# Kernel optimization log

Measured on AMD Instinct MI355X. Metric: run time of the kernel, lower is better.

The kernel has to match this reference:

```python
import jax, jax.numpy as jnp
import numpy as np

N = 2_000_000          # number of points
BOX = 4.0              # points live in [0, BOX)^3 meters
H = 3                  # hidden_channels (hardcoded in module)
NCLASS = 20
VS_ENC = [0.02, 0.04, 0.08]
VS_DEC = [0.08, 0.04, 0.02]


def _sparse_conv(feat, pts, vs, W, bias=None, transpose=False):
    """Voxel-hashed 3x3x3 sparse conv over continuous point positions.

    feat: [N, Cin] point features; pts: [N, 3] positions; W: [3,3,3,Cin,Cout].
    Points are voxelized at voxel size vs; each output point sums, over the 27
    kernel offsets, W[off] applied to the pooled features of the neighboring
    voxel.  transpose=True flips the kernel (SparseConvTranspose).
    """
    G = int(np.ceil(BOX / vs)) + 3                     # padded grid extent
    vox = jnp.floor(pts / vs).astype(jnp.int32) + 1    # +1 pad so offsets stay in range
    flat = (vox[:, 0] * G + vox[:, 1]) * G + vox[:, 2] # [N] flat voxel id
    Cin, Cout = W.shape[3], W.shape[4]
    # scatter-pool point features into the dense voxel grid
    grid = jnp.zeros((G * G * G, Cin), feat.dtype).at[flat].add(feat)
    Wk = (W[::-1, ::-1, ::-1] if transpose else W).reshape(27, Cin, Cout)
    out = jnp.zeros((feat.shape[0], Cout), feat.dtype)
    k = 0
    for dx in (-1, 0, 1):          # static 27-offset loop (kernel taps)
        for dy in (-1, 0, 1):
            for dz in (-1, 0, 1):
                nb = flat + (dx * G + dy) * G + dz
                out = out + grid[nb] @ Wk[k]
                k += 1
    if bias is not None:
        out = out + bias
    return out


def setup_inputs() -> dict:
    key = jax.random.key(0)
    ks = jax.random.split(key, 12)
    coords = jax.random.uniform(ks[0], (3, N), jnp.float32, 0.0, BOX)
    pixel_vals = jax.random.normal(ks[1], (N, 3), jnp.float32)
    w = lambda k: jax.random.normal(k, (3, 3, 3, H, H), jnp.float32) * 0.1
    return {
        "coords": coords,
        "pixel_vals": pixel_vals,
        "w_enc1": w(ks[2]),
        "w_enc2": w(ks[3]),
        "w_enc3": w(ks[4]),
        "w_dec1": w(ks[5]), "b_dec1": jnp.zeros((H,), jnp.float32),
        "w_dec2": w(ks[6]), "b_dec2": jnp.zeros((H,), jnp.float32),
        "w_dec3": w(ks[7]), "b_dec3": jnp.zeros((H,), jnp.float32),
        "w_gen": jax.random.normal(ks[8], (H, NCLASS), jnp.float32) * 0.1,
        "b_gen": jnp.zeros((NCLASS,), jnp.float32),
    }


def reference(coords, pixel_vals, w_enc1, w_enc2, w_enc3,
              w_dec1, b_dec1, w_dec2, b_dec2, w_dec3, b_dec3,
              w_gen, b_gen):
    pts = coords.T  # [N, 3]
    out = jax.nn.relu(_sparse_conv(pixel_vals, pts, VS_ENC[0], w_enc1))
    out = jax.nn.relu(_sparse_conv(out, pts, VS_ENC[1], w_enc2))
    out = jax.nn.relu(_sparse_conv(out, pts, VS_ENC[2], w_enc3))
    out = jax.nn.relu(_sparse_conv(out, pts, VS_DEC[0], w_dec1, b_dec1, transpose=True))
    out = jax.nn.relu(_sparse_conv(out, pts, VS_DEC[1], w_dec2, b_dec2, transpose=True))
    out = jax.nn.relu(_sparse_conv(out, pts, VS_DEC[2], w_dec3, b_dec3, transpose=True))
    return out @ w_gen + b_gen
```

## Files before the change

kernel.cpp:

```cpp
#include <hip/hip_runtime.h>
#include <math.h>


static constexpr int THREADS = 256;


__global__ void __launch_bounds__(THREADS)
scatter_pack_kernel(const float* __restrict__ coords, const float* __restrict__ pv,
                    int* __restrict__ flat, unsigned long long* __restrict__ gi, int n)
{
    int i = blockIdx.x * blockDim.x + threadIdx.x;
    if (i >= n) return;
    float x = coords[i], y = coords[n + i], z = coords[2 * n + i];
    int vx = (int)floorf(x * 50.0f) + 1;
    int vy = (int)floorf(y * 50.0f) + 1;
    int vz = (int)floorf(z * 50.0f) + 1;
    int f = (vx * 203 + vy) * 203 + vz;
    flat[i] = f;
    int q0 = __float2int_rn(pv[3 * i + 0] * 512.0f) + 4096;
    int q1 = __float2int_rn(pv[3 * i + 1] * 512.0f) + 4096;
    int q2 = __float2int_rn(pv[3 * i + 2] * 512.0f) + 4096;
    unsigned long long a = (1ULL << 48)
                         | ((unsigned long long)(unsigned int)q0 << 32)
                         | ((unsigned long long)(unsigned int)q1 << 16)
                         | (unsigned long long)(unsigned int)q2;
    atomicAdd(&gi[f], a);
}

__device__ __forceinline__ void dec16(unsigned long long v,
                                      float& f0, float& f1, float& f2)
{
    int cnt = (int)(v >> 48);
    int b = cnt << 12;
    f0 = (float)((int)((v >> 32) & 0xffff) - b) * (1.0f / 512.0f);
    f1 = (float)((int)((v >> 16) & 0xffff) - b) * (1.0f / 512.0f);
    f2 = (float)((int)(v         & 0xffff) - b) * (1.0f / 512.0f);
}

__global__ void __launch_bounds__(THREADS)
conv_gi_kernel(const unsigned long long* __restrict__ gi,
               const float* __restrict__ W,
               float4* __restrict__ T,
               unsigned char* __restrict__ cnt1)
{
    constexpr int G = 203, E = 201;
    __shared__ float sW[243];
    int t = threadIdx.x;
    if (t < 243) sW[t] = W[t];
    __syncthreads();

    int i = blockIdx.x * blockDim.x + t;
    if (i >= E * E * E) return;
    unsigned ui = (unsigned)i;
    int z = (int)(ui % (unsigned)E) + 1;  unsigned q = ui / (unsigned)E;
    int y = (int)(q % (unsigned)E) + 1;
    int x = (int)(q / (unsigned)E) + 1;
    int base = (x * G + y) * G + z;

    float a0 = 0.f, a1 = 0.f, a2 = 0.f;
    float cntC = 0.f;
    #pragma unroll
    for (int dx = -1; dx <= 1; ++dx) {
        #pragma unroll
        for (int dy = -1; dy <= 1; ++dy) {
            const unsigned long long* row = gi + base + (dx * G + dy) * G;
            unsigned long long vm = row[-1], v0 = row[0], vp = row[1];
            if (dx == 0 && dy == 0) cntC = (float)(int)(v0 >> 48);
            float m0, m1, m2, c0, c1, c2, p0, p1, p2;
            dec16(vm, m0, m1, m2);
            dec16(v0, c0, c1, c2);
            dec16(vp, p0, p1, p2);
            #pragma unroll
            for (int dz = -1; dz <= 1; ++dz) {
                const float* w = &sW[(((1 + dx) * 3 + (1 + dy)) * 3 + (1 + dz)) * 9];
                float g0 = (dz < 0) ? m0 : ((dz == 0) ? c0 : p0);
                float g1 = (dz < 0) ? m1 : ((dz == 0) ? c1 : p1);
                float g2 = (dz < 0) ? m2 : ((dz == 0) ? c2 : p2);
                a0 += g0 * w[0] + g1 * w[3] + g2 * w[6];
                a1 += g0 * w[1] + g1 * w[4] + g2 * w[7];
                a2 += g0 * w[2] + g1 * w[5] + g2 * w[8];
            }
        }
    }
    T[base] = make_float4(cntC, cntC * fmaxf(a0, 0.f),
                          cntC * fmaxf(a1, 0.f), cntC * fmaxf(a2, 0.f));
    cnt1[base] = (unsigned char)min((int)cntC, 255);
}

template <int G, int E, bool FLIP, bool MULC, bool BIAS>
__global__ void __launch_bounds__(THREADS)
conv_dense_kernel(const float4* __restrict__ in, const float* __restrict__ W,
                  const float* __restrict__ bias, float4* __restrict__ out)
{
    __shared__ float sW[243];
    __shared__ float sB[3];
    int t = threadIdx.x;
    if (t < 243) sW[t] = W[t];
    if (t < 3)   sB[t] = BIAS ? bias[t] : 0.0f;
    __syncthreads();

    int i = blockIdx.x * blockDim.x + t;
    if (i >= E * E * E) return;
    unsigned ui = (unsigned)i;
    int z = (int)(ui % (unsigned)E) + 1;  unsigned q = ui / (unsigned)E;
    int y = (int)(q % (unsigned)E) + 1;
    int x = (int)(q / (unsigned)E) + 1;
    int base = (x * G + y) * G + z;

    float a0 = sB[0], a1 = sB[1], a2 = sB[2];
    float cnt = 0.0f;
    #pragma unroll
    for (int dx = -1; dx <= 1; ++dx) {
        #pragma unroll
        for (int dy = -1; dy <= 1; ++dy) {
            int r = base + (dx * G + dy) * G;
            float4 va = in[r - 1], vb = in[r], vc = in[r + 1];
            if (dx == 0 && dy == 0) cnt = vb.x;
            #pragma unroll
            for (int dz = -1; dz <= 1; ++dz) {
                const int ax = FLIP ? 1 - dx : 1 + dx;
                const int ay = FLIP ? 1 - dy : 1 + dy;
                const int az = FLIP ? 1 - dz : 1 + dz;
                const float* w = &sW[((ax * 3 + ay) * 3 + az) * 9];
                float g0, g1, g2;
                if (dz == -1)      { g0 = va.y; g1 = va.z; g2 = va.w; }
                else if (dz == 0)  { g0 = vb.y; g1 = vb.z; g2 = vb.w; }
                else               { g0 = vc.y; g1 = vc.z; g2 = vc.w; }
                a0 += g0 * w[0] + g1 * w[3] + g2 * w[6];
                a1 += g0 * w[1] + g1 * w[4] + g2 * w[7];
                a2 += g0 * w[2] + g1 * w[5] + g2 * w[8];
            }
        }
    }
    a0 = fmaxf(a0, 0.0f); a1 = fmaxf(a1, 0.0f); a2 = fmaxf(a2, 0.0f);
    if (MULC) { a0 *= cnt; a1 *= cnt; a2 *= cnt; }
    out[base] = make_float4(cnt, a0, a1, a2);
}

template <int G, int GC, bool FLIP>
__global__ void __launch_bounds__(THREADS)
conv_fpar_kernel(const unsigned char* __restrict__ cnt,
                 const float4* __restrict__ coarse,
                 const float* __restrict__ W,
                 const float* __restrict__ bias,
                 float4* __restrict__ out)
{
    constexpr int E = G - 2;
    __shared__ float sW[243];
    __shared__ float sB[3];
    int t = threadIdx.x;
    if (t < 243) sW[t] = W[t];
    if (t < 3)   sB[t] = bias[t];
    __syncthreads();

    int i = blockIdx.x * blockDim.x + t;
    if (i >= E * E * E) return;
    unsigned ui = (unsigned)i;
    int z = (int)(ui % (unsigned)E) + 1;  unsigned q = ui / (unsigned)E;
    int y = (int)(q % (unsigned)E) + 1;
    int x = (int)(q / (unsigned)E) + 1;

    int pzm = ((z - 2) >> 1) + 1;
    int pz0 = ((z - 1) >> 1) + 1;
    int pzp = (z >> 1) + 1;

    float a0 = sB[0], a1 = sB[1], a2 = sB[2];
    float cnt_c = 0.0f;

    #pragma unroll
    for (int dx = -1; dx <= 1; ++dx) {
        int gxr = x + dx;
        int px = ((gxr - 1) >> 1) + 1;
        #pragma unroll
        for (int dy = -1; dy <= 1; ++dy) {
            int gyr = y + dy;
            int py = ((gyr - 1) >> 1) + 1;
            size_t r = ((size_t)gxr * G + gyr) * G + z;
            float cm = (float)cnt[r - 1];
            float c0 = (float)cnt[r];
            float cp = (float)cnt[r + 1];
            if (dx == 0 && dy == 0) cnt_c = c0;
            const float4* crow = coarse + ((size_t)px * GC + py) * GC;
            float4 Cm = crow[pzm], C0 = crow[pz0], Cp = crow[pzp];
            #pragma unroll
            for (int dz = -1; dz <= 1; ++dz) {
                float  cc = (dz < 0) ? cm : ((dz == 0) ? c0 : cp);
                float4 C  = (dz < 0) ? Cm : ((dz == 0) ? C0 : Cp);
                const int ax = FLIP ? 1 - dx : 1 + dx;
                const int ay = FLIP ? 1 - dy : 1 + dy;
                const int az = FLIP ? 1 - dz : 1 + dz;
                const float* w = &sW[((ax * 3 + ay) * 3 + az) * 9];
                float g0 = cc * C.y, g1 = cc * C.z, g2 = cc * C.w;
                a0 += g0 * w[0] + g1 * w[3] + g2 * w[6];
                a1 += g0 * w[1] + g1 * w[4] + g2 * w[7];
                a2 += g0 * w[2] + g1 * w[5] + g2 * w[8];
            }
        }
    }
    out[((size_t)x * G + y) * G + z] =
        make_float4(cnt_c, fmaxf(a0, 0.0f), fmaxf(a1, 0.0f), fmaxf(a2, 0.0f));
}

template <int Gc, int Gf, int Mc, bool WCNT>
__global__ void __launch_bounds__(THREADS)
down4_kernel(const float4* __restrict__ fine, float4* __restrict__ coarse,
             unsigned char* __restrict__ cntc)
{
    int i = blockIdx.x * blockDim.x + threadIdx.x;
    if (i >= Mc * Mc * Mc) return;
    unsigned ui = (unsigned)i;
    int zc = (int)(ui % (unsigned)Mc) + 1;  unsigned q = ui / (unsigned)Mc;
    int yc = (int)(q % (unsigned)Mc) + 1;
    int xc = (int)(q / (unsigned)Mc) + 1;
    int xf = 2 * xc - 1, yf = 2 * yc - 1, zf = 2 * zc - 1;
    float4 s = make_float4(0, 0, 0, 0);
    #pragma unroll
    for (int a = 0; a < 2; ++a)
        #pragma unroll
        for (int b = 0; b < 2; ++b) {
            int r = ((xf + a) * Gf + (yf + b)) * Gf + zf;
            float4 u = fine[r], v = fine[r + 1];
            s.x += u.x + v.x; s.y += u.y + v.y;
            s.z += u.z + v.z; s.w += u.w + v.w;
        }
    int idx = (xc * Gc + yc) * Gc + zc;
    coarse[idx] = s;
    if (WCNT) cntc[idx] = (unsigned char)min((int)(s.x + 0.5f), 255);
}

__global__ void __launch_bounds__(THREADS)
final_head_kernel(const int* __restrict__ flat, const float4* __restrict__ yF,
                  const float* __restrict__ wg, const float* __restrict__ bg,
                  float* __restrict__ out, int n)
{
    __shared__ float sG[60], sGB[20];
    int t = threadIdx.x;
    if (t < 60) sG[t] = wg[t];
    if (t < 20) sGB[t] = bg[t];
    __syncthreads();
    int i = blockIdx.x * blockDim.x + t;
    if (i >= n) return;
    float4 v = yF[flat[i]];
    float* o = out + (size_t)i * 20;
    #pragma unroll
    for (int c = 0; c < 20; ++c)
        o[c] = v.y * sG[c] + v.z * sG[20 + c] + v.w * sG[40 + c] + sGB[c];
}


__global__ void __launch_bounds__(THREADS)
voxelize_kernel(const float* __restrict__ coords, int* __restrict__ flat,
                float inv_vs, int G, int n)
{
    int i = blockIdx.x * blockDim.x + threadIdx.x;
    if (i >= n) return;
    int vx = (int)floorf(coords[i] * inv_vs) + 1;
    int vy = (int)floorf(coords[n + i] * inv_vs) + 1;
    int vz = (int)floorf(coords[2 * n + i] * inv_vs) + 1;
    flat[i] = (vx * G + vy) * G + vz;
}

__global__ void __launch_bounds__(THREADS)
scatter_kernel(const int* __restrict__ flat, const float* __restrict__ feat,
               float* __restrict__ grid, int n)
{
    int i = blockIdx.x * blockDim.x + threadIdx.x;
    if (i >= n) return;
    int f = flat[i];
    atomicAdd(&grid[3 * f + 0], feat[3 * i + 0]);
    atomicAdd(&grid[3 * f + 1], feat[3 * i + 1]);
    atomicAdd(&grid[3 * f + 2], feat[3 * i + 2]);
}

template <bool FLIP, bool FUSE_GEN>
__global__ void __launch_bounds__(THREADS)
gather_conv_kernel(const int* __restrict__ flat, const float* __restrict__ grid,
                   const float* __restrict__ W, const float* __restrict__ bias,
                   const float* __restrict__ w_gen, const float* __restrict__ b_gen,
                   float* __restrict__ out, int G, int n)
{
    __shared__ float sW[243];
    __shared__ float sB[3];
    __shared__ float sG[60];
    __shared__ float sGB[20];
    int t = threadIdx.x;
    if (t < 243) sW[t] = W[t];
    if (t < 3)   sB[t] = bias ? bias[t] : 0.0f;
    if (FUSE_GEN) {
        if (t < 60) sG[t]  = w_gen[t];
        if (t < 20) sGB[t] = b_gen[t];
    }
    __syncthreads();
    int i = blockIdx.x * blockDim.x + t;
    if (i >= n) return;
    int f = flat[i];
    float acc0 = sB[0], acc1 = sB[1], acc2 = sB[2];
    #pragma unroll
    for (int dx = -1; dx <= 1; ++dx) {
        #pragma unroll
        for (int dy = -1; dy <= 1; ++dy) {
            int base = f + (dx * G + dy) * G - 1;
            const float* g = &grid[3 * base];
            float gv[9];
            #pragma unroll
            for (int qq = 0; qq < 9; ++qq) gv[qq] = g[qq];
            #pragma unroll
            for (int dz = -1; dz <= 1; ++dz) {
                const int a = FLIP ? (1 - dx) : (1 + dx);
                const int b = FLIP ? (1 - dy) : (1 + dy);
                const int c = FLIP ? (1 - dz) : (1 + dz);
                const float* w = &sW[((a * 3 + b) * 3 + c) * 9];
                float g0 = gv[(dz + 1) * 3 + 0];
                float g1 = gv[(dz + 1) * 3 + 1];
                float g2 = gv[(dz + 1) * 3 + 2];
                acc0 += g0 * w[0] + g1 * w[3] + g2 * w[6];
                acc1 += g0 * w[1] + g1 * w[4] + g2 * w[7];
                acc2 += g0 * w[2] + g1 * w[5] + g2 * w[8];
            }
        }
    }
    acc0 = fmaxf(acc0, 0.0f); acc1 = fmaxf(acc1, 0.0f); acc2 = fmaxf(acc2, 0.0f);
    if (FUSE_GEN) {
        float* o = out + (size_t)i * 20;
        #pragma unroll
        for (int c = 0; c < 20; ++c)
            o[c] = acc0 * sG[c] + acc1 * sG[20 + c] + acc2 * sG[40 + c] + sGB[c];
    } else {
        out[3 * i + 0] = acc0;
        out[3 * i + 1] = acc1;
        out[3 * i + 2] = acc2;
    }
}

extern "C" void kernel_launch(void* const* d_in, const int* in_sizes, int n_in,
                              void* d_out, int out_size, void* d_ws, size_t ws_size,
                              hipStream_t stream)
{
    const float* coords     = (const float*)d_in[0];
    const float* pixel_vals = (const float*)d_in[1];
    const float* w_enc1 = (const float*)d_in[2];
    const float* w_enc2 = (const float*)d_in[3];
    const float* w_enc3 = (const float*)d_in[4];
    const float* w_dec1 = (const float*)d_in[5];
    const float* b_dec1 = (const float*)d_in[6];
    const float* w_dec2 = (const float*)d_in[7];
    const float* b_dec2 = (const float*)d_in[8];
    const float* w_dec3 = (const float*)d_in[9];
    const float* b_dec3 = (const float*)d_in[10];
    const float* w_gen  = (const float*)d_in[11];
    const float* b_gen  = (const float*)d_in[12];

    const int n = in_sizes[0] / 3;
    const int blocks = (n + THREADS - 1) / THREADS;
    float* out = (float*)d_out;

    constexpr size_t SZ_BIG1 = 33461712;
    constexpr size_t SZ_G2   = 4370912;
    constexpr size_t SZ_G3   = 595512;
    const size_t nf = ((size_t)n + 3) & ~(size_t)3;
    size_t off_flat = SZ_BIG1;
    size_t off_g2   = off_flat + nf;
    size_t off_t2   = off_g2 + SZ_G2;
    size_t off_g3   = off_t2 + SZ_G2;
    size_t off_t3   = off_g3 + SZ_G3;
    size_t need     = (off_t3 + SZ_G3) * 4;
    constexpr int    FTOT  = 203 * 203 * 203;
    constexpr int    C2TOT = 103 * 103 * 103;
    constexpr size_t GI_BYTES = (size_t)FTOT * 8;
    constexpr size_t CNT1_OFF = (GI_BYTES + 255) & ~(size_t)255;
    constexpr size_t CNT2_OFF = (CNT1_OFF + (size_t)FTOT + 255) & ~(size_t)255;
    const size_t outBytes = (size_t)out_size * 4;
    bool fast = (ws_size >= need) && (outBytes >= CNT2_OFF + (size_t)C2TOT);

    if (fast) {
        float* ws    = (float*)d_ws;
        float4* big1 = (float4*)ws;
        int*    flat = (int*)(ws + off_flat);
        float4* g2   = (float4*)(ws + off_g2);
        float4* t2   = (float4*)(ws + off_t2);
        float4* g3   = (float4*)(ws + off_g3);
        float4* t3   = (float4*)(ws + off_t3);
        unsigned long long* gi = (unsigned long long*)d_out;
        unsigned char* cnt1 = (unsigned char*)d_out + CNT1_OFF;
        unsigned char* cnt2 = (unsigned char*)d_out + CNT2_OFF;

        auto nb = [](int cells) { return (cells + THREADS - 1) / THREADS; };
        constexpr int C1 = 201 * 201 * 201, C2 = 101 * 101 * 101, C3 = 51 * 51 * 51;
        constexpr int D2 = 100 * 100 * 100, D3 = 50 * 50 * 50;

        (void)hipMemsetAsync(gi, 0, GI_BYTES, stream);
        (void)hipMemsetAsync(cnt1, 0, (size_t)FTOT, stream);
        (void)hipMemsetAsync(cnt2, 0, (size_t)C2TOT, stream);
        (void)hipMemsetAsync(g2, 0, SZ_G2 * 4, stream);
        (void)hipMemsetAsync(t2, 0, SZ_G2 * 4, stream);
        (void)hipMemsetAsync(g3, 0, SZ_G3 * 4, stream);
        (void)hipMemsetAsync(t3, 0, SZ_G3 * 4, stream);

        scatter_pack_kernel<<<blocks, THREADS, 0, stream>>>(
            coords, pixel_vals, flat, gi, n);

        conv_gi_kernel<<<nb(C1), THREADS, 0, stream>>>(gi, w_enc1, big1, cnt1);
        down4_kernel<103, 203, 100, true><<<nb(D2), THREADS, 0, stream>>>(big1, g2, cnt2);

        conv_dense_kernel<103, 101, false, true, false>
            <<<nb(C2), THREADS, 0, stream>>>(g2, w_enc2, nullptr, t2);
        down4_kernel<53, 103, 50, false><<<nb(D3), THREADS, 0, stream>>>(t2, g3, nullptr);

        conv_dense_kernel<53, 51, false, true, false>
            <<<nb(C3), THREADS, 0, stream>>>(g3, w_enc3, nullptr, t3);

        conv_dense_kernel<53, 51, true, false, true>
            <<<nb(C3), THREADS, 0, stream>>>(t3, w_dec1, b_dec1, g3);

        conv_fpar_kernel<103, 53, true>
            <<<nb(C2), THREADS, 0, stream>>>(cnt2, g3, w_dec2, b_dec2, t2);

        conv_fpar_kernel<203, 103, true>
            <<<nb(C1), THREADS, 0, stream>>>(cnt1, t2, w_dec3, b_dec3, big1);

        final_head_kernel<<<blocks, THREADS, 0, stream>>>(
            flat, big1, w_gen, b_gen, out, n);
        return;
    }

    float* ws   = (float*)d_ws;
    float* grid = ws;
    int*   flat = (int*)(ws + 25096284);
    float* featA = out;
    float* featB = out + (size_t)n * 3;

    const int   G1 = 203, G2 = 103, G3 = 53;
    const float I1 = 50.0f, I2 = 25.0f, I3 = 12.5f;
    auto gridBytes = [](int G) { return (size_t)G * G * G * 3 * sizeof(float); };

    voxelize_kernel<<<blocks, THREADS, 0, stream>>>(coords, flat, I1, G1, n);
    (void)hipMemsetAsync(grid, 0, gridBytes(G1), stream);
    scatter_kernel<<<blocks, THREADS, 0, stream>>>(flat, pixel_vals, grid, n);
    gather_conv_kernel<false, false><<<blocks, THREADS, 0, stream>>>(
        flat, grid, w_enc1, nullptr, nullptr, nullptr, featA, G1, n);

    voxelize_kernel<<<blocks, THREADS, 0, stream>>>(coords, flat, I2, G2, n);
    (void)hipMemsetAsync(grid, 0, gridBytes(G2), stream);
    scatter_kernel<<<blocks, THREADS, 0, stream>>>(flat, featA, grid, n);
    gather_conv_kernel<false, false><<<blocks, THREADS, 0, stream>>>(
        flat, grid, w_enc2, nullptr, nullptr, nullptr, featB, G2, n);

    voxelize_kernel<<<blocks, THREADS, 0, stream>>>(coords, flat, I3, G3, n);
    (void)hipMemsetAsync(grid, 0, gridBytes(G3), stream);
    scatter_kernel<<<blocks, THREADS, 0, stream>>>(flat, featB, grid, n);
    gather_conv_kernel<false, false><<<blocks, THREADS, 0, stream>>>(
        flat, grid, w_enc3, nullptr, nullptr, nullptr, featA, G3, n);

    (void)hipMemsetAsync(grid, 0, gridBytes(G3), stream);
    scatter_kernel<<<blocks, THREADS, 0, stream>>>(flat, featA, grid, n);
    gather_conv_kernel<true, false><<<blocks, THREADS, 0, stream>>>(
        flat, grid, w_dec1, b_dec1, nullptr, nullptr, featB, G3, n);

    voxelize_kernel<<<blocks, THREADS, 0, stream>>>(coords, flat, I2, G2, n);
    (void)hipMemsetAsync(grid, 0, gridBytes(G2), stream);
    scatter_kernel<<<blocks, THREADS, 0, stream>>>(flat, featB, grid, n);
    gather_conv_kernel<true, false><<<blocks, THREADS, 0, stream>>>(
        flat, grid, w_dec2, b_dec2, nullptr, nullptr, featA, G2, n);

    voxelize_kernel<<<blocks, THREADS, 0, stream>>>(coords, flat, I1, G1, n);
    (void)hipMemsetAsync(grid, 0, gridBytes(G1), stream);
    scatter_kernel<<<blocks, THREADS, 0, stream>>>(flat, featA, grid, n);
    gather_conv_kernel<true, true><<<blocks, THREADS, 0, stream>>>(
        flat, grid, w_dec3, b_dec3, w_gen, b_gen, out, G1, n);
}
```

Measured before the change: 527.2 us.

## Fuse final decoder conv with classification head, computed per point

The last transposed conv is no longer run over the whole 203^3 fine grid followed by a gather head. It is now evaluated only at each point's own voxel, inside the head kernel, which writes the 20 logits directly. This drops a dense grid pass of about 8M cells and its float4 write and read-back. In exchange, neighbouring points in the same voxel recompute the same 27-tap convolution, and the reads of cnt and coarse are now scattered. Buffers move so the fine-grid scratch T lives in the output buffer and gi, cnt1 and cnt2 move into the workspace.

Result: slower. 831.5 us (+57.7%).

```diff
diff --git a/kernel.cpp b/kernel.cpp
--- a/kernel.cpp
+++ b/kernel.cpp
@@ -201,6 +201,72 @@
         make_float4(cnt_c, fmaxf(a0, 0.0f), fmaxf(a1, 0.0f), fmaxf(a2, 0.0f));
 }
 
+__global__ void __launch_bounds__(THREADS)
+fused_dec3_head_kernel(const int* __restrict__ flat,
+                       const unsigned char* __restrict__ cnt,
+                       const float4* __restrict__ coarse,
+                       const float* __restrict__ W,
+                       const float* __restrict__ bias,
+                       const float* __restrict__ wg, const float* __restrict__ bg,
+                       float* __restrict__ out, int n)
+{
+    constexpr int G = 203, GC = 103;
+    __shared__ float sW[243];
+    __shared__ float sB[3];
+    __shared__ float sG[60], sGB[20];
+    int t = threadIdx.x;
+    if (t < 243) sW[t] = W[t];
+    if (t < 3)   sB[t] = bias[t];
+    if (t < 60)  sG[t] = wg[t];
+    if (t < 20)  sGB[t] = bg[t];
+    __syncthreads();
+
+    int i = blockIdx.x * blockDim.x + t;
+    if (i >= n) return;
+    int f = flat[i];
+    int z = f % G;  int rq = f / G;
+    int y = rq % G; int x = rq / G;
+
+    int pzm = ((z - 2) >> 1) + 1;
+    int pz0 = ((z - 1) >> 1) + 1;
+    int pzp = (z >> 1) + 1;
+
+    float a0 = sB[0], a1 = sB[1], a2 = sB[2];
+
+    #pragma unroll
+    for (int dx = -1; dx <= 1; ++dx) {
+        int gxr = x + dx;
+        int px = ((gxr - 1) >> 1) + 1;
+        #pragma unroll
+        for (int dy = -1; dy <= 1; ++dy) {
+            int gyr = y + dy;
+            int py = ((gyr - 1) >> 1) + 1;
+            size_t r = ((size_t)gxr * G + gyr) * G + z;
+            float cm = (float)cnt[r - 1];
+            float c0 = (float)cnt[r];
+            float cp = (float)cnt[r + 1];
+            const float4* crow = coarse + ((size_t)px * GC + py) * GC;
+            float4 Cm = crow[pzm], C0 = crow[pz0], Cp = crow[pzp];
+            #pragma unroll
+            for (int dz = -1; dz <= 1; ++dz) {
+                float  cc = (dz < 0) ? cm : ((dz == 0) ? c0 : cp);
+                float4 C  = (dz < 0) ? Cm : ((dz == 0) ? C0 : Cp);
+                const int ax = 1 - dx, ay = 1 - dy, az = 1 - dz;
+                const float* w = &sW[((ax * 3 + ay) * 3 + az) * 9];
+                float g0 = cc * C.y, g1 = cc * C.z, g2 = cc * C.w;
+                a0 += g0 * w[0] + g1 * w[3] + g2 * w[6];
+                a1 += g0 * w[1] + g1 * w[4] + g2 * w[7];
+                a2 += g0 * w[2] + g1 * w[5] + g2 * w[8];
+            }
+        }
+    }
+    a0 = fmaxf(a0, 0.0f); a1 = fmaxf(a1, 0.0f); a2 = fmaxf(a2, 0.0f);
+    float* o = out + (size_t)i * 20;
+    #pragma unroll
+    for (int c = 0; c < 20; ++c)
+        o[c] = a0 * sG[c] + a1 * sG[20 + c] + a2 * sG[40 + c] + sGB[c];
+}
+
 template <int Gc, int Gf, int Mc, bool WCNT>
 __global__ void __launch_bounds__(THREADS)
 down4_kernel(const float4* __restrict__ fine, float4* __restrict__ coarse,
@@ -226,25 +292,6 @@
     int idx = (xc * Gc + yc) * Gc + zc;
     coarse[idx] = s;
     if (WCNT) cntc[idx] = (unsigned char)min((int)(s.x + 0.5f), 255);
-}
-
-__global__ void __launch_bounds__(THREADS)
-final_head_kernel(const int* __restrict__ flat, const float4* __restrict__ yF,
-                  const float* __restrict__ wg, const float* __restrict__ bg,
-                  float* __restrict__ out, int n)
-{
-    __shared__ float sG[60], sGB[20];
-    int t = threadIdx.x;
-    if (t < 60) sG[t] = wg[t];
-    if (t < 20) sGB[t] = bg[t];
-    __syncthreads();
-    int i = blockIdx.x * blockDim.x + t;
-    if (i >= n) return;
-    float4 v = yF[flat[i]];
-    float* o = out + (size_t)i * 20;
-    #pragma unroll
-    for (int c = 0; c < 20; ++c)
-        o[c] = v.y * sG[c] + v.z * sG[20 + c] + v.w * sG[40 + c] + sGB[c];
 }
 
 
@@ -354,53 +401,53 @@
     const int blocks = (n + THREADS - 1) / THREADS;
     float* out = (float*)d_out;
 
-    constexpr size_t SZ_BIG1 = 33461712;
-    constexpr size_t SZ_G2   = 4370912;
-    constexpr size_t SZ_G3   = 595512;
-    const size_t nf = ((size_t)n + 3) & ~(size_t)3;
-    size_t off_flat = SZ_BIG1;
-    size_t off_g2   = off_flat + nf;
-    size_t off_t2   = off_g2 + SZ_G2;
-    size_t off_g3   = off_t2 + SZ_G2;
-    size_t off_t3   = off_g3 + SZ_G3;
-    size_t need     = (off_t3 + SZ_G3) * 4;
-    constexpr int    FTOT  = 203 * 203 * 203;
-    constexpr int    C2TOT = 103 * 103 * 103;
-    constexpr size_t GI_BYTES = (size_t)FTOT * 8;
-    constexpr size_t CNT1_OFF = (GI_BYTES + 255) & ~(size_t)255;
-    constexpr size_t CNT2_OFF = (CNT1_OFF + (size_t)FTOT + 255) & ~(size_t)255;
+    constexpr int FTOT  = 203 * 203 * 203;
+    constexpr int C2TOT = 103 * 103 * 103;
+    constexpr int C3TOT = 53 * 53 * 53;
+
+    auto al = [](size_t v) { return (v + 255) & ~(size_t)255; };
+    size_t o_gi   = 0;
+    size_t o_cnt1 = al(o_gi + (size_t)FTOT * 8);
+    size_t o_cnt2 = al(o_cnt1 + (size_t)FTOT);
+    size_t o_flat = al(o_cnt2 + (size_t)C2TOT);
+    size_t o_g2   = al(o_flat + (size_t)n * 4);
+    size_t o_t2   = al(o_g2 + (size_t)C2TOT * 16);
+    size_t o_g3   = al(o_t2 + (size_t)C2TOT * 16);
+    size_t o_t3   = al(o_g3 + (size_t)C3TOT * 16);
+    size_t need   = al(o_t3 + (size_t)C3TOT * 16);
     const size_t outBytes = (size_t)out_size * 4;
-    bool fast = (ws_size >= need) && (outBytes >= CNT2_OFF + (size_t)C2TOT);
+    const size_t T_BYTES  = (size_t)FTOT * 16;
+    bool fast = (ws_size >= need) && (outBytes >= T_BYTES);
 
     if (fast) {
-        float* ws    = (float*)d_ws;
-        float4* big1 = (float4*)ws;
-        int*    flat = (int*)(ws + off_flat);
-        float4* g2   = (float4*)(ws + off_g2);
-        float4* t2   = (float4*)(ws + off_t2);
-        float4* g3   = (float4*)(ws + off_g3);
-        float4* t3   = (float4*)(ws + off_t3);
-        unsigned long long* gi = (unsigned long long*)d_out;
-        unsigned char* cnt1 = (unsigned char*)d_out + CNT1_OFF;
-        unsigned char* cnt2 = (unsigned char*)d_out + CNT2_OFF;
+        char* ws = (char*)d_ws;
+        unsigned long long* gi = (unsigned long long*)(ws + o_gi);
+        unsigned char* cnt1 = (unsigned char*)(ws + o_cnt1);
+        unsigned char* cnt2 = (unsigned char*)(ws + o_cnt2);
+        int*    flat = (int*)(ws + o_flat);
+        float4* g2   = (float4*)(ws + o_g2);
+        float4* t2   = (float4*)(ws + o_t2);
+        float4* g3   = (float4*)(ws + o_g3);
+        float4* t3   = (float4*)(ws + o_t3);
+        float4* T    = (float4*)d_out;
 
         auto nb = [](int cells) { return (cells + THREADS - 1) / THREADS; };
         constexpr int C1 = 201 * 201 * 201, C2 = 101 * 101 * 101, C3 = 51 * 51 * 51;
         constexpr int D2 = 100 * 100 * 100, D3 = 50 * 50 * 50;
 
-        (void)hipMemsetAsync(gi, 0, GI_BYTES, stream);
+        (void)hipMemsetAsync(gi, 0, (size_t)FTOT * 8, stream);
         (void)hipMemsetAsync(cnt1, 0, (size_t)FTOT, stream);
         (void)hipMemsetAsync(cnt2, 0, (size_t)C2TOT, stream);
-        (void)hipMemsetAsync(g2, 0, SZ_G2 * 4, stream);
-        (void)hipMemsetAsync(t2, 0, SZ_G2 * 4, stream);
-        (void)hipMemsetAsync(g3, 0, SZ_G3 * 4, stream);
-        (void)hipMemsetAsync(t3, 0, SZ_G3 * 4, stream);
+        (void)hipMemsetAsync(g2, 0, (size_t)C2TOT * 16, stream);
+        (void)hipMemsetAsync(t2, 0, (size_t)C2TOT * 16, stream);
+        (void)hipMemsetAsync(g3, 0, (size_t)C3TOT * 16, stream);
+        (void)hipMemsetAsync(t3, 0, (size_t)C3TOT * 16, stream);
 
         scatter_pack_kernel<<<blocks, THREADS, 0, stream>>>(
             coords, pixel_vals, flat, gi, n);
 
-        conv_gi_kernel<<<nb(C1), THREADS, 0, stream>>>(gi, w_enc1, big1, cnt1);
-        down4_kernel<103, 203, 100, true><<<nb(D2), THREADS, 0, stream>>>(big1, g2, cnt2);
+        conv_gi_kernel<<<nb(C1), THREADS, 0, stream>>>(gi, w_enc1, T, cnt1);
+        down4_kernel<103, 203, 100, true><<<nb(D2), THREADS, 0, stream>>>(T, g2, cnt2);
 
         conv_dense_kernel<103, 101, false, true, false>
             <<<nb(C2), THREADS, 0, stream>>>(g2, w_enc2, nullptr, t2);
@@ -415,17 +462,14 @@
         conv_fpar_kernel<103, 53, true>
             <<<nb(C2), THREADS, 0, stream>>>(cnt2, g3, w_dec2, b_dec2, t2);
 
-        conv_fpar_kernel<203, 103, true>
-            <<<nb(C1), THREADS, 0, stream>>>(cnt1, t2, w_dec3, b_dec3, big1);
-
-        final_head_kernel<<<blocks, THREADS, 0, stream>>>(
-            flat, big1, w_gen, b_gen, out, n);
+        fused_dec3_head_kernel<<<blocks, THREADS, 0, stream>>>(
+            flat, cnt1, t2, w_dec3, b_dec3, w_gen, b_gen, out, n);
         return;
     }
 
-    float* ws   = (float*)d_ws;
-    float* grid = ws;
-    int*   flat = (int*)(ws + 25096284);
+    float* fws  = (float*)d_ws;
+    float* grid = fws;
+    int*   flat = (int*)(fws + 25096284);
     float* featA = out;
     float* featB = out + (size_t)n * 3;
 
```
